# Performance work log

Measured on AMD Instinct MI355X. Metric: run time of the kernel, lower is better.

The kernel has to match this reference:

```python
import jax, jax.numpy as jnp
import numpy as np

TEMPERATURE = 0.5
EPS = 1e-8  # torch CosineSimilarity eps


def setup_inputs() -> dict:
    key = jax.random.key(0)
    k1, k2 = jax.random.split(key)
    B, D = 4096, 256
    return {
        "z_i": jax.random.normal(k1, (B, D), dtype=jnp.float32),
        "z_j": jax.random.normal(k2, (B, D), dtype=jnp.float32),
    }


def reference(z_i, z_j):
    B = z_i.shape[0]
    N = 2 * B
    z = jnp.concatenate([z_i, z_j], axis=0)  # [N, D]
    # cosine similarity == normalized dot product (eps-clamped norms like torch)
    norms = jnp.maximum(jnp.linalg.norm(z, axis=1, keepdims=True), EPS)
    zn = z / norms
    sim = jnp.matmul(zn, zn.T) / TEMPERATURE  # [N, N]

    idx = jnp.arange(B)
    # positives: diag(sim, +B) and diag(sim, -B)
    pos = jnp.concatenate([sim[idx, idx + B], sim[idx + B, idx]])  # [N]

    # CrossEntropy with label 0 over [pos_i, negatives_i] reduces to
    # logsumexp over row i excluding the self-diagonal, minus pos_i.
    r = jnp.arange(N)
    neg_inf = jnp.finfo(sim.dtype).min
    sim_masked = jnp.where(r[:, None] == r[None, :], neg_inf, sim)
    lse = jax.nn.logsumexp(sim_masked, axis=1)  # [N]

    loss = (jnp.sum(lse) - jnp.sum(pos)) / N
    return loss
```

## Files before the change

### kernel.cpp

```cpp
#include <hip/hip_runtime.h>
#include <cstdint>

#define B_ROWS 4096
#define N_ROWS 8192
#define D_DIM  256
#define BT     128
#define TGRID  64
#define NTILES 2080

typedef __attribute__((ext_vector_type(4))) float f32x4;
typedef __attribute__((ext_vector_type(2))) unsigned long u64x2;

__device__ __forceinline__ void gload16(const void* g, void* l) {
    __builtin_amdgcn_global_load_lds(
        (const __attribute__((address_space(1))) void*)g,
        (__attribute__((address_space(3))) void*)l, 16, 0, 0);
}

__device__ __forceinline__ f32x4 exp4(f32x4 v) {
    f32x4 r;
    r.x = __expf(v.x); r.y = __expf(v.y); r.z = __expf(v.z); r.w = __expf(v.w);
    return r;
}

__device__ __forceinline__ unsigned f2e4m3(float f) {
    union { float f; unsigned u; } v; v.f = f;
    unsigned s = (v.u >> 24) & 0x80u;
    unsigned mag = v.u & 0x7fffffffu;
    int e = (int)(mag >> 23) - 127;
    if (e >= -6) {
        unsigned r = mag + 0x7ffffu + ((mag >> 20) & 1u);
        int e2 = (int)(r >> 23) - 127;
        unsigned m3 = (r >> 20) & 7u;
        return s | (unsigned)((e2 + 7) << 3) | m3;
    }
    if (e < -10) return s;
    float q = rintf(fabsf(f) * 512.0f);
    unsigned qi = (unsigned)q;
    return s | qi;
}

__global__ __launch_bounds__(256) void normpos_kernel(const float* __restrict__ zi,
                                                      const float* __restrict__ zj,
                                                      unsigned char* __restrict__ zn,
                                                      float* __restrict__ pospartial) {
    int wid = threadIdx.x >> 6;
    int lane = threadIdx.x & 63;
    int p = blockIdx.x * 4 + wid;
    f32x4 ga = *(const f32x4*)(zi + (size_t)p * D_DIM + lane * 4);
    f32x4 gb = *(const f32x4*)(zj + (size_t)p * D_DIM + lane * 4);
    float sa = ga.x * ga.x + ga.y * ga.y + ga.z * ga.z + ga.w * ga.w;
    float sb = gb.x * gb.x + gb.y * gb.y + gb.z * gb.z + gb.w * gb.w;
    #pragma unroll
    for (int m = 1; m < 64; m <<= 1) { sa += __shfl_xor(sa, m, 64); sb += __shfl_xor(sb, m, 64); }
    float fa = 1.41421356237309515f / fmaxf(sqrtf(sa), 1e-8f);
    float fb = 1.41421356237309515f / fmaxf(sqrtf(sb), 1e-8f);
    f32x4 na, nb;
    na.x = ga.x * fa; na.y = ga.y * fa; na.z = ga.z * fa; na.w = ga.w * fa;
    nb.x = gb.x * fb; nb.y = gb.y * fb; nb.z = gb.z * fb; nb.w = gb.w * fb;
    unsigned pa = f2e4m3(na.x) | (f2e4m3(na.y) << 8) | (f2e4m3(na.z) << 16) | (f2e4m3(na.w) << 24);
    unsigned pb = f2e4m3(nb.x) | (f2e4m3(nb.y) << 8) | (f2e4m3(nb.z) << 16) | (f2e4m3(nb.w) << 24);
    int bytepos = (lane >> 4) * 64 + ((lane >> 1) & 3) * 16 + ((lane >> 3) & 1) * 8 + 4 * (lane & 1);
    *(unsigned*)(zn + (size_t)p * 256 + bytepos) = pa;
    *(unsigned*)(zn + (size_t)(p + B_ROWS) * 256 + bytepos) = pb;
    float d = na.x * nb.x + na.y * nb.y + na.z * nb.z + na.w * nb.w;
    #pragma unroll
    for (int m = 1; m < 64; m <<= 1) d += __shfl_xor(d, m, 64);
    if (lane == 0) pospartial[p] = d;
}

__global__ __launch_bounds__(256, 2) void simclr_gemm_kernel(const unsigned char* __restrict__ zn,
                                                             float* __restrict__ P) {
    __shared__ unsigned char As[4 * 8192];
    __shared__ unsigned char Bs[4 * 8192];
    __shared__ float rPpart[2][BT];
    __shared__ float cPpart[2][BT];

    const int tid = threadIdx.x;
    const int lane = tid & 63, wid = tid >> 6;
    const int wr = wid >> 1, wc = wid & 1;

    int bid = (int)((blockIdx.x & 7) * (NTILES / 8) + (blockIdx.x >> 3));
    int ti = (int)((129.0f - sqrtf(16641.0f - 8.0f * (float)bid)) * 0.5f);
    while ((ti + 1) * TGRID - ((ti + 1) * ti) / 2 <= bid) ++ti;
    while (ti * TGRID - (ti * (ti - 1)) / 2 > bid) --ti;
    const int tj = ti + (bid - (ti * TGRID - (ti * (ti - 1)) / 2));

    const char* gA = (const char*)zn + (size_t)ti * BT * 256;
    const char* gB = (const char*)zn + (size_t)tj * BT * 256;

    const int r0 = tid >> 2;
    const int sch = (tid & 3) ^ ((tid >> 3) & 3);
    const unsigned lo = (unsigned)tid * 16;

    #pragma unroll
    for (int g = 0; g < 4; ++g) {
        #pragma unroll
        for (int h = 0; h < 2; ++h) {
            size_t go = (size_t)(h * 64 + r0) * 256 + (size_t)g * 64 + (size_t)sch * 16;
            gload16(gA + go, &As[g * 8192 + h * 4096 + lo]);
            gload16(gB + go, &Bs[g * 8192 + h * 4096 + lo]);
        }
    }

    f32x4 acc[4][4];
    #pragma unroll
    for (int m = 0; m < 4; ++m)
        #pragma unroll
        for (int n = 0; n < 4; ++n)
            acc[m][n] = (f32x4){0.f, 0.f, 0.f, 0.f};

    const int ysw = (lane >> 4) ^ (((lane & 15) >> 1) & 3);
    const int arow = wr * 64 + (lane & 15);
    const int brow = wc * 64 + (lane & 15);

    __syncthreads();

    #pragma unroll
    for (int g = 0; g < 4; ++g) {
        u64x2 af[4], bfr[4];
        #pragma unroll
        for (int m = 0; m < 4; ++m)
            af[m] = *(const u64x2*)&As[g * 8192 + (arow + m * 16) * 64 + ysw * 16];
        #pragma unroll
        for (int n = 0; n < 4; ++n)
            bfr[n] = *(const u64x2*)&Bs[g * 8192 + (brow + n * 16) * 64 + ysw * 16];
        #pragma unroll
        for (int m = 0; m < 4; ++m)
            #pragma unroll
            for (int n = 0; n < 4; ++n) {
                acc[m][n] = __builtin_amdgcn_mfma_f32_16x16x32_fp8_fp8(
                    (long)af[m].x, (long)bfr[n].x, acc[m][n], 0, 0, 0);
                acc[m][n] = __builtin_amdgcn_mfma_f32_16x16x32_fp8_fp8(
                    (long)af[m].y, (long)bfr[n].y, acc[m][n], 0, 0, 0);
            }
    }

    float cs[4] = {0.f, 0.f, 0.f, 0.f};
    #pragma unroll
    for (int m = 0; m < 4; ++m) {
        f32x4 ef[4];
        #pragma unroll
        for (int n = 0; n < 4; ++n) ef[n] = exp4(acc[m][n]);
        f32x4 rv = ef[0] + ef[1] + ef[2] + ef[3];
        #pragma unroll
        for (int msk = 1; msk <= 8; msk <<= 1) {
            rv.x += __shfl_xor(rv.x, msk, 64);
            rv.y += __shfl_xor(rv.y, msk, 64);
            rv.z += __shfl_xor(rv.z, msk, 64);
            rv.w += __shfl_xor(rv.w, msk, 64);
        }
        if ((lane & 15) == 0) {
            int rbase = wr * 64 + m * 16 + (lane >> 4) * 4;
            rPpart[wc][rbase + 0] = rv.x;
            rPpart[wc][rbase + 1] = rv.y;
            rPpart[wc][rbase + 2] = rv.z;
            rPpart[wc][rbase + 3] = rv.w;
        }
        #pragma unroll
        for (int n = 0; n < 4; ++n)
            cs[n] += ef[n].x + ef[n].y + ef[n].z + ef[n].w;
    }
    #pragma unroll
    for (int n = 0; n < 4; ++n) {
        float c = cs[n];
        c += __shfl_xor(c, 16, 64);
        c += __shfl_xor(c, 32, 64);
        if (lane < 16) cPpart[wr][wc * 64 + n * 16 + lane] = c;
    }
    __syncthreads();

    if (tid < BT) {
        P[(size_t)tj * N_ROWS + ti * BT + tid] = rPpart[0][tid] + rPpart[1][tid];
    } else if (ti != tj) {
        int t = tid - BT;
        P[(size_t)ti * N_ROWS + tj * BT + t] = cPpart[0][t] + cPpart[1][t];
    }
}

__global__ __launch_bounds__(256) void reduce_rows_kernel(const float* __restrict__ P,
                                                          const float* __restrict__ pospartial,
                                                          float* __restrict__ blockpart) {
    const float E2 = 7.38905609893065f;
    int row = blockIdx.x * 256 + threadIdx.x;
    float s = 0.f;
    #pragma unroll 16
    for (int src = 0; src < TGRID; ++src)
        s += P[(size_t)src * N_ROWS + row];
    float v = logf(s - E2);
    if (threadIdx.x < 128)
        v -= 2.0f * pospartial[blockIdx.x * 128 + threadIdx.x];
    #pragma unroll
    for (int m = 1; m < 64; m <<= 1) v += __shfl_xor(v, m, 64);
    __shared__ float ws[4];
    if ((threadIdx.x & 63) == 0) ws[threadIdx.x >> 6] = v;
    __syncthreads();
    if (threadIdx.x == 0) blockpart[blockIdx.x] = ws[0] + ws[1] + ws[2] + ws[3];
}

__global__ __launch_bounds__(64) void final_kernel(const float* __restrict__ blockpart,
                                                   float* __restrict__ out) {
    int lane = threadIdx.x;
    float v = (lane < 32) ? blockpart[lane] : 0.f;
    #pragma unroll
    for (int m = 1; m < 64; m <<= 1) v += __shfl_xor(v, m, 64);
    if (lane == 0) out[0] = v / (float)N_ROWS;
}

extern "C" void kernel_launch(void* const* d_in, const int* in_sizes, int n_in,
                              void* d_out, int out_size, void* d_ws, size_t ws_size,
                              hipStream_t stream) {
    const float* zi = (const float*)d_in[0];
    const float* zj = (const float*)d_in[1];
    char* ws = (char*)d_ws;
    unsigned char* zn = (unsigned char*)ws;
    float* P = (float*)(ws + 2 * 1024 * 1024);
    float* pospartial = (float*)(ws + 4 * 1024 * 1024);
    float* blockpart = (float*)(ws + 4 * 1024 * 1024 + 16 * 1024);

    normpos_kernel<<<B_ROWS / 4, 256, 0, stream>>>(zi, zj, zn, pospartial);
    simclr_gemm_kernel<<<NTILES, 256, 0, stream>>>(zn, P);
    reduce_rows_kernel<<<N_ROWS / 256, 256, 0, stream>>>(P, pospartial, blockpart);
    final_kernel<<<1, 64, 0, stream>>>(blockpart, (float*)d_out);
}
```

Before: 40.95 us.

## Restructure GEMM into persistent row-panel waves streaming column panels from global

Replaces the 2080 one-tile-per-block launch over 128x128 triangular tiles with 512 blocks. Each wave keeps a 64-row A panel in registers and loops over 64-wide column panels in strides of 32, reading B fragments straight from global memory with no LDS staging or barriers. Paired row panels p and 127-p balance the triangular work. Row sums accumulate in registers and column sums are written per panel, with the reduce kernel adjusted to read both buffers. This cuts LDS traffic and launch count, at the cost of uncoalesced global fragment loads and a variable-length column sum loop in the reduction.

```diff
diff --git a/kernel.cpp b/kernel.cpp
--- a/kernel.cpp
+++ b/kernel.cpp
@@ -4,18 +4,11 @@
 #define B_ROWS 4096
 #define N_ROWS 8192
 #define D_DIM  256
-#define BT     128
-#define TGRID  64
-#define NTILES 2080
+#define NPAN   128
+#define NBLK   512
 
 typedef __attribute__((ext_vector_type(4))) float f32x4;
 typedef __attribute__((ext_vector_type(2))) unsigned long u64x2;
-
-__device__ __forceinline__ void gload16(const void* g, void* l) {
-    __builtin_amdgcn_global_load_lds(
-        (const __attribute__((address_space(1))) void*)g,
-        (__attribute__((address_space(3))) void*)l, 16, 0, 0);
-}
 
 __device__ __forceinline__ f32x4 exp4(f32x4 v) {
     f32x4 r;
@@ -70,126 +63,111 @@
 }
 
 __global__ __launch_bounds__(256, 2) void simclr_gemm_kernel(const unsigned char* __restrict__ zn,
-                                                             float* __restrict__ P) {
-    __shared__ unsigned char As[4 * 8192];
-    __shared__ unsigned char Bs[4 * 8192];
-    __shared__ float rPpart[2][BT];
-    __shared__ float cPpart[2][BT];
-
+                                                             float* __restrict__ Prow,
+                                                             float* __restrict__ Pcol) {
     const int tid = threadIdx.x;
     const int lane = tid & 63, wid = tid >> 6;
-    const int wr = wid >> 1, wc = wid & 1;
-
-    int bid = (int)((blockIdx.x & 7) * (NTILES / 8) + (blockIdx.x >> 3));
-    int ti = (int)((129.0f - sqrtf(16641.0f - 8.0f * (float)bid)) * 0.5f);
-    while ((ti + 1) * TGRID - ((ti + 1) * ti) / 2 <= bid) ++ti;
-    while (ti * TGRID - (ti * (ti - 1)) / 2 > bid) --ti;
-    const int tj = ti + (bid - (ti * TGRID - (ti * (ti - 1)) / 2));
-
-    const char* gA = (const char*)zn + (size_t)ti * BT * 256;
-    const char* gB = (const char*)zn + (size_t)tj * BT * 256;
-
-    const int r0 = tid >> 2;
-    const int sch = (tid & 3) ^ ((tid >> 3) & 3);
-    const unsigned lo = (unsigned)tid * 16;
-
-    #pragma unroll
-    for (int g = 0; g < 4; ++g) {
+    const int p = (int)blockIdx.x >> 3;
+    const int c = (int)blockIdx.x & 7;
+    const int s = c * 4 + wid;
+    const int l15 = lane & 15, lq = lane >> 4;
+
+    #pragma unroll
+    for (int half = 0; half < 2; ++half) {
+        const int r = half ? (127 - p) : p;
+        const char* gA = (const char*)zn + (size_t)r * 64 * 256;
+
+        u64x2 af[4][4];
         #pragma unroll
-        for (int h = 0; h < 2; ++h) {
-            size_t go = (size_t)(h * 64 + r0) * 256 + (size_t)g * 64 + (size_t)sch * 16;
-            gload16(gA + go, &As[g * 8192 + h * 4096 + lo]);
-            gload16(gB + go, &Bs[g * 8192 + h * 4096 + lo]);
+        for (int m = 0; m < 4; ++m)
+            #pragma unroll
+            for (int g = 0; g < 4; ++g)
+                af[m][g] = *(const u64x2*)(gA + (size_t)(m * 16 + l15) * 256 + g * 64 + lq * 16);
+
+        f32x4 rs[4];
+        #pragma unroll
+        for (int m = 0; m < 4; ++m) rs[m] = (f32x4){0.f, 0.f, 0.f, 0.f};
+
+        for (int cx = r + s; cx < NPAN; cx += 32) {
+            const char* gB = (const char*)zn + (size_t)cx * 64 * 256;
+            f32x4 acc[4][4];
+            #pragma unroll
+            for (int m = 0; m < 4; ++m)
+                #pragma unroll
+                for (int n = 0; n < 4; ++n)
+                    acc[m][n] = (f32x4){0.f, 0.f, 0.f, 0.f};
+
+            #pragma unroll
+            for (int g = 0; g < 4; ++g) {
+                u64x2 bfr[4];
+                #pragma unroll
+                for (int n = 0; n < 4; ++n)
+                    bfr[n] = *(const u64x2*)(gB + (size_t)(n * 16 + l15) * 256 + g * 64 + lq * 16);
+                #pragma unroll
+                for (int m = 0; m < 4; ++m)
+                    #pragma unroll
+                    for (int n = 0; n < 4; ++n) {
+                        acc[m][n] = __builtin_amdgcn_mfma_f32_16x16x32_fp8_fp8(
+                            (long)af[m][g].x, (long)bfr[n].x, acc[m][n], 0, 0, 0);
+                        acc[m][n] = __builtin_amdgcn_mfma_f32_16x16x32_fp8_fp8(
+                            (long)af[m][g].y, (long)bfr[n].y, acc[m][n], 0, 0, 0);
+                    }
+            }
+
+            float cs[4] = {0.f, 0.f, 0.f, 0.f};
+            #pragma unroll
+            for (int m = 0; m < 4; ++m) {
+                f32x4 ef[4];
+                #pragma unroll
+                for (int n = 0; n < 4; ++n) ef[n] = exp4(acc[m][n]);
+                f32x4 rv = ef[0] + ef[1] + ef[2] + ef[3];
+                #pragma unroll
+                for (int msk = 1; msk <= 8; msk <<= 1) {
+                    rv.x += __shfl_xor(rv.x, msk, 64);
+                    rv.y += __shfl_xor(rv.y, msk, 64);
+                    rv.z += __shfl_xor(rv.z, msk, 64);
+                    rv.w += __shfl_xor(rv.w, msk, 64);
+                }
+                rs[m] += rv;
+                #pragma unroll
+                for (int n = 0; n < 4; ++n)
+                    cs[n] += ef[n].x + ef[n].y + ef[n].z + ef[n].w;
+            }
+            if (cx != r) {
+                #pragma unroll
+                for (int n = 0; n < 4; ++n) {
+                    float cc = cs[n];
+                    cc += __shfl_xor(cc, 16, 64);
+                    cc += __shfl_xor(cc, 32, 64);
+                    if (lane < 16)
+                        Pcol[(size_t)r * N_ROWS + cx * 64 + n * 16 + lane] = cc;
+                }
+            }
+        }
+
+        if (l15 == 0) {
+            #pragma unroll
+            for (int m = 0; m < 4; ++m)
+                *(f32x4*)&Prow[(size_t)s * N_ROWS + r * 64 + m * 16 + lq * 4] = rs[m];
         }
     }
-
-    f32x4 acc[4][4];
-    #pragma unroll
-    for (int m = 0; m < 4; ++m)
-        #pragma unroll
-        for (int n = 0; n < 4; ++n)
-            acc[m][n] = (f32x4){0.f, 0.f, 0.f, 0.f};
-
-    const int ysw = (lane >> 4) ^ (((lane & 15) >> 1) & 3);
-    const int arow = wr * 64 + (lane & 15);
-    const int brow = wc * 64 + (lane & 15);
-
-    __syncthreads();
-
-    #pragma unroll
-    for (int g = 0; g < 4; ++g) {
-        u64x2 af[4], bfr[4];
-        #pragma unroll
-        for (int m = 0; m < 4; ++m)
-            af[m] = *(const u64x2*)&As[g * 8192 + (arow + m * 16) * 64 + ysw * 16];
-        #pragma unroll
-        for (int n = 0; n < 4; ++n)
-            bfr[n] = *(const u64x2*)&Bs[g * 8192 + (brow + n * 16) * 64 + ysw * 16];
-        #pragma unroll
-        for (int m = 0; m < 4; ++m)
-            #pragma unroll
-            for (int n = 0; n < 4; ++n) {
-                acc[m][n] = __builtin_amdgcn_mfma_f32_16x16x32_fp8_fp8(
-                    (long)af[m].x, (long)bfr[n].x, acc[m][n], 0, 0, 0);
-                acc[m][n] = __builtin_amdgcn_mfma_f32_16x16x32_fp8_fp8(
-                    (long)af[m].y, (long)bfr[n].y, acc[m][n], 0, 0, 0);
-            }
-    }
-
-    float cs[4] = {0.f, 0.f, 0.f, 0.f};
-    #pragma unroll
-    for (int m = 0; m < 4; ++m) {
-        f32x4 ef[4];
-        #pragma unroll
-        for (int n = 0; n < 4; ++n) ef[n] = exp4(acc[m][n]);
-        f32x4 rv = ef[0] + ef[1] + ef[2] + ef[3];
-        #pragma unroll
-        for (int msk = 1; msk <= 8; msk <<= 1) {
-            rv.x += __shfl_xor(rv.x, msk, 64);
-            rv.y += __shfl_xor(rv.y, msk, 64);
-            rv.z += __shfl_xor(rv.z, msk, 64);
-            rv.w += __shfl_xor(rv.w, msk, 64);
-        }
-        if ((lane & 15) == 0) {
-            int rbase = wr * 64 + m * 16 + (lane >> 4) * 4;
-            rPpart[wc][rbase + 0] = rv.x;
-            rPpart[wc][rbase + 1] = rv.y;
-            rPpart[wc][rbase + 2] = rv.z;
-            rPpart[wc][rbase + 3] = rv.w;
-        }
-        #pragma unroll
-        for (int n = 0; n < 4; ++n)
-            cs[n] += ef[n].x + ef[n].y + ef[n].z + ef[n].w;
-    }
-    #pragma unroll
-    for (int n = 0; n < 4; ++n) {
-        float c = cs[n];
-        c += __shfl_xor(c, 16, 64);
-        c += __shfl_xor(c, 32, 64);
-        if (lane < 16) cPpart[wr][wc * 64 + n * 16 + lane] = c;
-    }
-    __syncthreads();
-
-    if (tid < BT) {
-        P[(size_t)tj * N_ROWS + ti * BT + tid] = rPpart[0][tid] + rPpart[1][tid];
-    } else if (ti != tj) {
-        int t = tid - BT;
-        P[(size_t)ti * N_ROWS + tj * BT + t] = cPpart[0][t] + cPpart[1][t];
-    }
-}
-
-__global__ __launch_bounds__(256) void reduce_rows_kernel(const float* __restrict__ P,
+}
+
+__global__ __launch_bounds__(256) void reduce_rows_kernel(const float* __restrict__ Prow,
+                                                          const float* __restrict__ Pcol,
                                                           const float* __restrict__ pospartial,
                                                           float* __restrict__ blockpart) {
     const float E2 = 7.38905609893065f;
     int row = blockIdx.x * 256 + threadIdx.x;
-    float s = 0.f;
-    #pragma unroll 16
-    for (int src = 0; src < TGRID; ++src)
-        s += P[(size_t)src * N_ROWS + row];
-    float v = logf(s - E2);
-    if (threadIdx.x < 128)
-        v -= 2.0f * pospartial[blockIdx.x * 128 + threadIdx.x];
+    int cx = row >> 6;
+    float ssum = 0.f;
+    #pragma unroll 8
+    for (int s = 0; s < 32; ++s)
+        ssum += Prow[(size_t)s * N_ROWS + row];
+    for (int rr = 0; rr < cx; ++rr)
+        ssum += Pcol[(size_t)rr * N_ROWS + row];
+    float v = logf(ssum - E2);
+    if (row < B_ROWS) v -= 2.0f * pospartial[row];
     #pragma unroll
     for (int m = 1; m < 64; m <<= 1) v += __shfl_xor(v, m, 64);
     __shared__ float ws[4];
@@ -214,12 +192,13 @@
     const float* zj = (const float*)d_in[1];
     char* ws = (char*)d_ws;
     unsigned char* zn = (unsigned char*)ws;
-    float* P = (float*)(ws + 2 * 1024 * 1024);
-    float* pospartial = (float*)(ws + 4 * 1024 * 1024);
-    float* blockpart = (float*)(ws + 4 * 1024 * 1024 + 16 * 1024);
+    float* Prow = (float*)(ws + 2 * 1024 * 1024);
+    float* Pcol = (float*)(ws + 3 * 1024 * 1024);
+    float* pospartial = (float*)(ws + 7 * 1024 * 1024);
+    float* blockpart = (float*)(ws + 7 * 1024 * 1024 + 16 * 1024);
 
     normpos_kernel<<<B_ROWS / 4, 256, 0, stream>>>(zi, zj, zn, pospartial);
-    simclr_gemm_kernel<<<NTILES, 256, 0, stream>>>(zn, P);
-    reduce_rows_kernel<<<N_ROWS / 256, 256, 0, stream>>>(P, pospartial, blockpart);
+    simclr_gemm_kernel<<<NBLK, 256, 0, stream>>>(zn, Prow, Pcol);
+    reduce_rows_kernel<<<N_ROWS / 256, 256, 0, stream>>>(Prow, Pcol, pospartial, blockpart);
     final_kernel<<<1, 64, 0, stream>>>(blockpart, (float*)d_out);
 }
```

Result: slower. 76.80 us (+87.5%).
